# Kernel optimization log

Measured on AMD Instinct MI355X. Metric: run time of the kernel, lower is better.

The kernel has to match this reference:

```python
import jax, jax.numpy as jnp
import numpy as np

EPS = 1e-6        # vn_layers EPS
BN_EPS = 1e-5     # torch BatchNorm eps
NEG = 0.2         # leaky relu negative_slope


def _bcast(v, nd):
    return v.reshape((1, -1) + (1,) * (nd - 2))


def vn_linear_leaky(x, W, D, gamma, beta):
    """VNLinearLeakyReLU: x [B,Cin,3,...], W/D [Cout,Cin] -> [B,Cout,3,...]."""
    p = jnp.einsum('oc,bcv...->bov...', W, x)
    # VNBatchNorm (training-mode batch statistics) on vector norms
    norm = jnp.linalg.norm(p, axis=2) + EPS              # [B,Cout,...]
    axes = (0,) + tuple(range(2, norm.ndim))
    mu = jnp.mean(norm, axis=axes, keepdims=True)
    var = jnp.mean((norm - mu) ** 2, axis=axes, keepdims=True)
    norm_bn = (norm - mu) / jnp.sqrt(var + BN_EPS)
    norm_bn = norm_bn * _bcast(gamma, norm.ndim) + _bcast(beta, norm.ndim)
    p = p / norm[:, :, None] * norm_bn[:, :, None]
    # VN LeakyReLU against learned direction d
    d = jnp.einsum('oc,bcv...->bov...', D, x)
    dot = jnp.sum(p * d, axis=2, keepdims=True)
    mask = (dot >= 0).astype(p.dtype)
    dns = jnp.sum(d * d, axis=2, keepdims=True)
    return NEG * p + (1 - NEG) * (mask * p + (1 - mask) * (p - (dot / (dns + EPS)) * d))


def chnorm(x):
    """channel_equi_vec_normalize: x [B,C,3,...]."""
    n = jnp.linalg.norm(x, axis=2, keepdims=True)        # [B,C,1,...]
    x_dir = x / jnp.maximum(n, 1e-12)
    n_ch = jnp.linalg.norm(n, axis=1, keepdims=True)     # normalize norms over channels
    return x_dir * (n / jnp.maximum(n_ch, 1e-12))


def get_graph_feature(y, k):
    """VN-DGCNN graph feature: y [B,C,3,N] -> [B,2C,3,N,K]."""
    B, C, _, N = y.shape
    yp = jnp.transpose(y, (0, 3, 1, 2))                  # [B,N,C,3]
    flat = yp.reshape(B, N, 3 * C)
    sq = jnp.sum(flat * flat, axis=-1)                   # [B,N]
    inner = jnp.einsum('bnd,bmd->bnm', flat, flat)
    neg_dist = 2 * inner - sq[:, :, None] - sq[:, None, :]
    _, idx = jax.lax.top_k(neg_dist, k)                  # [B,N,K] nearest (incl. self)
    nbr = jax.vmap(lambda pts, ids: pts[ids])(yp, idx)   # [B,N,K,C,3]
    ctr = jnp.broadcast_to(yp[:, :, None], (B, N, k, C, 3))
    feat = jnp.concatenate([nbr - ctr, ctr], axis=3)     # [B,N,K,2C,3]
    return jnp.transpose(feat, (0, 3, 4, 1, 2))


def reference(x, y, Wq, Dq, gq, bq, Wk, Dk, gk, bk, Wv, Dv, gv, bv, k):
    Qx = chnorm(vn_linear_leaky(x, Wq, Dq, gq, bq))      # [B,C,3,N]
    yg = get_graph_feature(y, k)                         # [B,2C,3,N,K]
    Ky = chnorm(vn_linear_leaky(yg, Wk, Dk, gk, bk))     # [B,C,3,N,K]
    Vy = vn_linear_leaky(yg, Wv, Dv, gv, bv)             # [B,C,3,N,K]
    qk = jnp.sum(Ky * Qx[..., None], axis=2)             # [B,C,N,K]
    C = qk.shape[1]
    atten = jax.nn.softmax(qk / jnp.sqrt(jnp.float32(3 * C)), axis=-1)
    return x + jnp.sum(atten[:, :, None] * Vy, axis=-1)  # [B,C,3,N]


def setup_inputs() -> dict:
    key = jax.random.key(0)
    B, C, N, K = 4, 64, 2048, 16
    ks = jax.random.split(key, 8)
    s1 = 1.0 / np.sqrt(C)
    s2 = 1.0 / np.sqrt(2 * C)
    return {
        'x': jax.random.normal(ks[0], (B, C, 3, N), jnp.float32),
        'y': jax.random.normal(ks[1], (B, C, 3, N), jnp.float32),
        'Wq': jax.random.normal(ks[2], (C, C), jnp.float32) * s1,
        'Dq': jax.random.normal(ks[3], (C, C), jnp.float32) * s1,
        'gq': jnp.ones((C,), jnp.float32),
        'bq': jnp.zeros((C,), jnp.float32),
        'Wk': jax.random.normal(ks[4], (C, 2 * C), jnp.float32) * s2,
        'Dk': jax.random.normal(ks[5], (C, 2 * C), jnp.float32) * s2,
        'gk': jnp.ones((C,), jnp.float32),
        'bk': jnp.zeros((C,), jnp.float32),
        'Wv': jax.random.normal(ks[6], (C, 2 * C), jnp.float32) * s2,
        'Dv': jax.random.normal(ks[7], (C, 2 * C), jnp.float32) * s2,
        'gv': jnp.ones((C,), jnp.float32),
        'bv': jnp.zeros((C,), jnp.float32),
        'k': K,
    }
```

## Files before the change

### kernel.cpp

```cpp
#include <hip/hip_runtime.h>
#include <cstdint>
#include <cstddef>

constexpr int B_ = 4, C_ = 64, N_ = 2048, K_ = 16;
constexpr int D3 = 192;
constexpr float EPS_ = 1e-6f, BNE_ = 1e-5f, NEG_ = 0.2f;
constexpr size_t S_ = (size_t)B_ * N_ * D3;

constexpr size_t OFF_PQ  = 0;
constexpr size_t OFF_DQ  = 1*S_;
constexpr size_t OFF_GB  = 2*S_;
constexpr size_t OFF_WK  = 6*S_;
constexpr size_t OFF_WDK = 7*S_;
constexpr size_t OFF_WV  = 8*S_;
constexpr size_t OFF_WDV = 9*S_;
constexpr size_t OFF_SQ  = 10*S_;
constexpr size_t OFF_ST  = OFF_SQ + (size_t)B_*N_;
constexpr size_t OFF_IDX = OFF_ST + 1024;
constexpr size_t OFF_DIST= OFF_IDX + (size_t)B_*N_*K_;

__device__ __forceinline__ float wred_sum(float v) {
  #pragma unroll
  for (int off = 32; off > 0; off >>= 1) v += __shfl_xor(v, off, 64);
  return v;
}

__device__ __forceinline__ void gld_lds16(const float* g, float* l) {
  __builtin_amdgcn_global_load_lds(
      (const __attribute__((address_space(1))) void*)g,
      (__attribute__((address_space(3))) void*)l, 16, 0, 0);
}

__device__ __forceinline__ void vnlk(float& p0, float& p1, float& p2,
                                     float d0, float d1, float d2,
                                     float s, float sh) {
  float n2 = p0*p0 + p1*p1 + p2*p2;
  float norm = __builtin_amdgcn_sqrtf(n2) + EPS_;
  float f = fmaf(norm, s, sh) * __builtin_amdgcn_rcpf(norm);
  p0 *= f; p1 *= f; p2 *= f;
  float dot = p0*d0 + p1*d1 + p2*d2;
  float dns = d0*d0 + d1*d1 + d2*d2;
  float g = (1.f - NEG_) * fminf(dot, 0.f) * __builtin_amdgcn_rcpf(dns + EPS_);
  p0 = fmaf(-g, d0, p0); p1 = fmaf(-g, d1, p1); p2 = fmaf(-g, d2, p2);
}

__device__ __forceinline__ float chnorm_sc(float nc, float nch) {
  return nc * __builtin_amdgcn_rcpf(fmaxf(nc, 1e-12f))
            * __builtin_amdgcn_rcpf(fmaxf(nch, 1e-12f));
}

template<bool PAIR>
__device__ __forceinline__ void do_mm(const float (*ys)[36], const float (*Wl)[129],
                                      float* __restrict__ out0, float* __restrict__ out1,
                                      float* s1s, float* s2s, bool qs,
                                      int og, int ng, int b, int n0, int rs0) {
  float accU[4][2][3] = {};
  float accW[4][2][3] = {};
  #pragma unroll 4
  for (int c = 0; c < 64; ++c) {
    float w1[4], wd[4];
    #pragma unroll
    for (int i = 0; i < 4; ++i) {
      w1[i] = Wl[og*4 + i][c];
      if (PAIR) wd[i] = Wl[og*4 + i][64 + c] - w1[i];
    }
    #pragma unroll
    for (int jj = 0; jj < 2; ++jj)
      #pragma unroll
      for (int v = 0; v < 3; ++v) {
        float yv = ys[c*3 + v][ng*2 + jj];
        #pragma unroll
        for (int i = 0; i < 4; ++i) {
          accU[i][jj][v] = fmaf(w1[i], yv, accU[i][jj][v]);
          if (PAIR) accW[i][jj][v] = fmaf(wd[i], yv, accW[i][jj][v]);
        }
      }
  }
  #pragma unroll
  for (int jj = 0; jj < 2; ++jj) {
    int n = n0 + ng*2 + jj;
    size_t base0 = ((size_t)b*N_ + n)*rs0 + og*12;
    alignas(16) float tmp[12];
    #pragma unroll
    for (int i = 0; i < 4; ++i)
      #pragma unroll
      for (int v = 0; v < 3; ++v) tmp[i*3+v] = accU[i][jj][v];
    float4* dst = (float4*)(out0 + base0);
    dst[0] = ((float4*)tmp)[0]; dst[1] = ((float4*)tmp)[1]; dst[2] = ((float4*)tmp)[2];
    if (PAIR) {
      size_t base1 = ((size_t)b*N_ + n)*D3 + og*12;
      #pragma unroll
      for (int i = 0; i < 4; ++i)
        #pragma unroll
        for (int v = 0; v < 3; ++v) tmp[i*3+v] = accW[i][jj][v];
      float4* dst1 = (float4*)(out1 + base1);
      dst1[0] = ((float4*)tmp)[0]; dst1[1] = ((float4*)tmp)[1]; dst1[2] = ((float4*)tmp)[2];
    }
  }
  if (!PAIR && qs) {
    #pragma unroll
    for (int i = 0; i < 4; ++i) {
      float a = 0.f, b2 = 0.f;
      #pragma unroll
      for (int jj = 0; jj < 2; ++jj) {
        float nn = sqrtf(accU[i][jj][0]*accU[i][jj][0] + accU[i][jj][1]*accU[i][jj][1]
                       + accU[i][jj][2]*accU[i][jj][2]) + EPS_;
        a += nn; b2 += nn*nn;
      }
      atomicAdd(&s1s[og*4 + i], a);
      atomicAdd(&s2s[og*4 + i], b2);
    }
  }
}

__global__ __launch_bounds__(256) void transform_kernel(
    const float* __restrict__ x, const float* __restrict__ y,
    const float* __restrict__ Wq, const float* __restrict__ Dq,
    const float* __restrict__ Wk, const float* __restrict__ Dk,
    const float* __restrict__ Wv, const float* __restrict__ Dv,
    float* __restrict__ ws) {
  __shared__ float ys[D3][36];
  __shared__ float Wl[64][129];
  __shared__ float s1s[64], s2s[64];
  int t = threadIdx.x, n0 = blockIdx.x*32, b = blockIdx.y, z = blockIdx.z;
  const bool isx = (z < 2);
  const float* in = (isx ? x : y) + (size_t)b*D3*N_;
  #pragma unroll
  for (int i = 0; i < 6; ++i) {
    int lin = t + i*256;
    int d = lin >> 3, c4 = (lin & 7)*4;
    *(float4*)&ys[d][c4] = *(const float4*)&in[(size_t)d*N_ + n0 + c4];
  }
  const float* Wg = (z==0)?Wq:(z==1)?Dq:(z==2)?Wk:(z==3)?Dk:(z==4)?Wv:Dv;
  if (isx) { for (int i = t; i < 4096; i += 256) Wl[i>>6][i&63] = Wg[i]; }
  else     { for (int i = t; i < 8192; i += 256) Wl[i>>7][i&127] = Wg[i]; }
  if (z == 0 && t < 64) { s1s[t] = 0.f; s2s[t] = 0.f; }
  __syncthreads();
  if (z == 2 && t < 32) {
    float s = 0.f;
    for (int d = 0; d < D3; ++d) { float v = ys[d][t]; s += v*v; }
    ws[OFF_SQ + (size_t)b*N_ + n0 + t] = s;
  }
  int og = t & 15, ng = t >> 4;
  float* st = ws + OFF_ST;
  if (isx) {
    float* out0 = ws + (z ? OFF_DQ : OFF_PQ);
    do_mm<false>(ys, Wl, out0, nullptr, s1s, s2s, z == 0, og, ng, b, n0, D3);
    if (z == 0) {
      __syncthreads();
      if (t < 64) { atomicAdd(&st[t], s1s[t]); atomicAdd(&st[64 + t], s2s[t]); }
    }
  } else {
    int seg = z - 2;
    float* out0 = ws + OFF_GB + (size_t)seg*192;
    float* out1 = ws + ((z==2)?OFF_WK:(z==3)?OFF_WDK:(z==4)?OFF_WV:OFF_WDV);
    do_mm<true>(ys, Wl, out0, out1, nullptr, nullptr, false, og, ng, b, n0, 768);
  }
}

__global__ __launch_bounds__(256) void dist_kernel(const float* __restrict__ y,
                                                   float* __restrict__ ws,
                                                   int b0, size_t dstride) {
  __shared__ float As[2][2048];
  __shared__ float Bs[2][4096];
  int b = b0 + blockIdx.z;
  const float* yb = y + (size_t)b * D3 * N_;
  const float* sq = ws + OFF_SQ + (size_t)b * N_;
  float* dist = ws + OFF_DIST + dstride * blockIdx.z;
  int t = threadIdx.x;
  int m0 = blockIdx.x * 256, n0 = blockIdx.y * 128;
  int tm = t & 15, tn = t >> 4;

  auto stage = [&](int buf, int dt) {
    #pragma unroll
    for (int j = 0; j < 2; ++j) {
      int idx = j*256 + t;
      gld_lds16(&yb[(size_t)(dt*16 + (idx >> 5))*N_ + n0 + (idx & 31)*4],
                &As[buf][idx*4]);
    }
    #pragma unroll
    for (int j = 0; j < 4; ++j) {
      int idx = j*256 + t;
      gld_lds16(&yb[(size_t)(dt*16 + (idx >> 6))*N_ + m0 + (idx & 63)*4],
                &Bs[buf][idx*4]);
    }
  };

  float acc[8][16] = {};
  stage(0, 0);
  __syncthreads();
  int cur = 0;
  for (int dt = 0; dt < 12; ++dt) {
    if (dt < 11) stage(cur ^ 1, dt + 1);
    const float* Ac = As[cur];
    const float* Bc = Bs[cur];
    #pragma unroll 4
    for (int dd = 0; dd < 16; ++dd) {
      float4 a0 = *(const float4*)&Ac[dd*128 + tn*4];
      float4 a1 = *(const float4*)&Ac[dd*128 + 64 + tn*4];
      float4 b0 = *(const float4*)&Bc[dd*256 + tm*4];
      float4 b1 = *(const float4*)&Bc[dd*256 + 64 + tm*4];
      float4 b2 = *(const float4*)&Bc[dd*256 + 128 + tm*4];
      float4 b3 = *(const float4*)&Bc[dd*256 + 192 + tm*4];
      float an[8] = {a0.x, a0.y, a0.z, a0.w, a1.x, a1.y, a1.z, a1.w};
      float bm[16] = {b0.x, b0.y, b0.z, b0.w, b1.x, b1.y, b1.z, b1.w,
                      b2.x, b2.y, b2.z, b2.w, b3.x, b3.y, b3.z, b3.w};
      #pragma unroll
      for (int j = 0; j < 8; ++j)
        #pragma unroll
        for (int i = 0; i < 16; ++i)
          acc[j][i] = fmaf(an[j], bm[i], acc[j][i]);
    }
    __syncthreads();
    cur ^= 1;
  }
  float smv[16];
  #pragma unroll
  for (int r = 0; r < 4; ++r) {
    float4 s4 = *(const float4*)&sq[m0 + r*64 + tm*4];
    smv[r*4+0] = s4.x; smv[r*4+1] = s4.y; smv[r*4+2] = s4.z; smv[r*4+3] = s4.w;
  }
  #pragma unroll
  for (int j = 0; j < 8; ++j) {
    int n = n0 + ((j < 4) ? (tn*4 + j) : (64 + tn*4 + j - 4));
    float sn = sq[n];
    size_t rowb = (size_t)n*N_ + m0 + tm*4;
    #pragma unroll
    for (int r = 0; r < 4; ++r) {
      float4 rr;
      rr.x = 2.f*acc[j][r*4+0] - sn - smv[r*4+0];
      rr.y = 2.f*acc[j][r*4+1] - sn - smv[r*4+1];
      rr.z = 2.f*acc[j][r*4+2] - sn - smv[r*4+2];
      rr.w = 2.f*acc[j][r*4+3] - sn - smv[r*4+3];
      *(float4*)&dist[rowb + r*64] = rr;
    }
  }
}

__global__ __launch_bounds__(256) void topk_kernel(const float* __restrict__ ws_c,
                                                   int* __restrict__ idxo,
                                                   int b0, size_t dstride) {
  int t = threadIdx.x;
  int w = t >> 6, l = t & 63;
  int n = blockIdx.x*4 + w;
  int b = b0 + blockIdx.y;
  const float* dr = ws_c + OFF_DIST + dstride*blockIdx.y + (size_t)n * N_;
  float v[32];
  #pragma unroll
  for (int j = 0; j < 32; ++j) v[j] = dr[j*64 + l];
  int mine = 0;
  for (int it = 0; it < K_; ++it) {
    float bv = v[0]; int bj = 0;
    #pragma unroll
    for (int j = 1; j < 32; ++j) {
      bool g = v[j] > bv;
      bv = g ? v[j] : bv;
      bj = g ? j : bj;
    }
    int bm = bj*64 + l;
    #pragma unroll
    for (int off = 32; off > 0; off >>= 1) {
      float ov = __shfl_xor(bv, off, 64);
      int   om = __shfl_xor(bm, off, 64);
      if (ov > bv || (ov == bv && om < bm)) { bv = ov; bm = om; }
    }
    if (l == it) mine = bm;
    int wj = bm >> 6, wl = bm & 63;
    #pragma unroll
    for (int j = 0; j < 32; ++j)
      v[j] = (j == wj && l == wl) ? -3.4e38f : v[j];
  }
  if (l < K_) idxo[((size_t)b*N_ + n)*K_ + l] = mine;
}

__global__ __launch_bounds__(256) void kvstats_kernel(float* __restrict__ ws,
                                                      const int* __restrict__ idxp) {
  int t = threadIdx.x, o = t & 63, eg = t >> 6;
  int e0 = blockIdx.x * 128, b = blockIdx.y;
  const float* GB = ws + OFF_GB;
  const float* wK = ws + OFF_WK; const float* wV = ws + OFF_WV;
  int bN = b * N_;
  float k1 = 0.f, k2 = 0.f, v1 = 0.f, v2 = 0.f;
  for (int j = 0; j < 32; ++j) {
    int e = e0 + eg + j*4;
    int n = e >> 4, kk = e & 15;
    int m = idxp[(bN + n)*K_ + kk];
    int rb = (bN + n)*D3 + o*3;
    size_t gb = (size_t)(bN + m)*768 + o*3;
    float p0 = GB[gb] + wK[rb], p1 = GB[gb+1] + wK[rb+1], p2 = GB[gb+2] + wK[rb+2];
    float nk = __builtin_amdgcn_sqrtf(p0*p0 + p1*p1 + p2*p2) + EPS_;
    k1 += nk; k2 += nk*nk;
    float q0 = GB[gb+384] + wV[rb], q1 = GB[gb+385] + wV[rb+1], q2 = GB[gb+386] + wV[rb+2];
    float nv = __builtin_amdgcn_sqrtf(q0*q0 + q1*q1 + q2*q2) + EPS_;
    v1 += nv; v2 += nv*nv;
  }
  __shared__ float red[4][256];
  red[0][t] = k1; red[1][t] = k2; red[2][t] = v1; red[3][t] = v2;
  __syncthreads();
  if (t < 64) {
    float* st = ws + OFF_ST;
    float a = red[0][t] + red[0][t+64] + red[0][t+128] + red[0][t+192];
    atomicAdd(&st[128 + t], a);
    a = red[1][t] + red[1][t+64] + red[1][t+128] + red[1][t+192];
    atomicAdd(&st[192 + t], a);
    a = red[2][t] + red[2][t+64] + red[2][t+128] + red[2][t+192];
    atomicAdd(&st[256 + t], a);
    a = red[3][t] + red[3][t+64] + red[3][t+128] + red[3][t+192];
    atomicAdd(&st[320 + t], a);
  }
}

__global__ __launch_bounds__(256, 2) void final_kernel(const float* __restrict__ x,
                                                       const float* __restrict__ ws_c,
                                                       const int* __restrict__ idxp,
                                                       const float* __restrict__ gq,
                                                       const float* __restrict__ bq,
                                                       const float* __restrict__ gk,
                                                       const float* __restrict__ bk,
                                                       const float* __restrict__ gv,
                                                       const float* __restrict__ bv,
                                                       float* __restrict__ out) {
  const float* pq  = ws_c + OFF_PQ;  const float* dq  = ws_c + OFF_DQ;
  const float* GB  = ws_c + OFF_GB;
  const float* wK  = ws_c + OFF_WK;  const float* wDk = ws_c + OFF_WDK;
  const float* wV  = ws_c + OFF_WV;  const float* wDv = ws_c + OFF_WDV;
  const float* st  = ws_c + OFF_ST;
  int t = threadIdx.x, o = t & 63, w = t >> 6;
  int n0 = blockIdx.x*4, n = n0 + w, b = blockIdx.y;
  int bN = b * N_;
  __shared__ float ob2[192][5];
  float sQ, shQ, sK, shK, sV, shV;
  {
    const float icq = 1.f / (float)(B_ * N_);
    float mu = st[o] * icq;
    float var = fmaxf(st[64+o]*icq - mu*mu, 0.f);
    sQ = gq[o] * rsqrtf(var + BNE_); shQ = bq[o] - mu*sQ;
    const float ick = 1.f / (float)(B_ * N_ * K_);
    mu = st[128+o] * ick;
    var = fmaxf(st[192+o]*ick - mu*mu, 0.f);
    sK = gk[o] * rsqrtf(var + BNE_); shK = bk[o] - mu*sK;
    mu = st[256+o] * ick;
    var = fmaxf(st[320+o]*ick - mu*mu, 0.f);
    sV = gv[o] * rsqrtf(var + BNE_); shV = bv[o] - mu*sV;
  }
  int mi[16];
  {
    const int* ip = idxp + (size_t)(bN + n)*K_;
    int4 a0 = *(const int4*)&ip[0];  mi[0]=a0.x;  mi[1]=a0.y;  mi[2]=a0.z;  mi[3]=a0.w;
    int4 a1 = *(const int4*)&ip[4];  mi[4]=a1.x;  mi[5]=a1.y;  mi[6]=a1.z;  mi[7]=a1.w;
    int4 a2 = *(const int4*)&ip[8];  mi[8]=a2.x;  mi[9]=a2.y;  mi[10]=a2.z; mi[11]=a2.w;
    int4 a3 = *(const int4*)&ip[12]; mi[12]=a3.x; mi[13]=a3.y; mi[14]=a3.z; mi[15]=a3.w;
  }
  int rb = (bN + n)*D3 + o*3;
  float q0 = pq[rb], q1 = pq[rb+1], q2 = pq[rb+2];
  float e0 = dq[rb], e1 = dq[rb+1], e2 = dq[rb+2];
  vnlk(q0, q1, q2, e0, e1, e2, sQ, shQ);
  float qn2 = q0*q0 + q1*q1 + q2*q2;
  float qsc = chnorm_sc(__builtin_amdgcn_sqrtf(qn2),
                        __builtin_amdgcn_sqrtf(wred_sum(qn2)));
  float qx0 = q0*qsc, qx1 = q1*qsc, qx2 = q2*qsc;
  float wk0 = wK[rb],  wk1 = wK[rb+1],  wk2 = wK[rb+2];
  float wdk0= wDk[rb], wdk1= wDk[rb+1], wdk2= wDk[rb+2];
  const float isq = 0.07216878364870323f;
  float qk[16];
  #pragma unroll
  for (int kk = 0; kk < 16; ++kk) {
    size_t gb = (size_t)(bN + mi[kk])*768 + o*3;
    float p0 = GB[gb]     + wk0, p1 = GB[gb+1]   + wk1, p2 = GB[gb+2]   + wk2;
    float f0 = GB[gb+192] + wdk0, f1 = GB[gb+193] + wdk1, f2 = GB[gb+194] + wdk2;
    vnlk(p0, p1, p2, f0, f1, f2, sK, shK);
    float nc2 = p0*p0 + p1*p1 + p2*p2;
    float sc = chnorm_sc(__builtin_amdgcn_sqrtf(nc2),
                         __builtin_amdgcn_sqrtf(wred_sum(nc2)));
    qk[kk] = (p0*qx0 + p1*qx1 + p2*qx2) * (sc * isq);
  }
  float mx = qk[0];
  #pragma unroll
  for (int kk = 1; kk < 16; ++kk) mx = fmaxf(mx, qk[kk]);
  float se = 0.f;
  #pragma unroll
  for (int kk = 0; kk < 16; ++kk) { float e = __expf(qk[kk] - mx); qk[kk] = e; se += e; }
  float inv = __builtin_amdgcn_rcpf(se);
  float wv0 = wV[rb],  wv1 = wV[rb+1],  wv2 = wV[rb+2];
  float wdv0= wDv[rb], wdv1= wDv[rb+1], wdv2= wDv[rb+2];
  float a0 = 0.f, a1 = 0.f, a2 = 0.f;
  #pragma unroll
  for (int kk = 0; kk < 16; ++kk) {
    size_t gb = (size_t)(bN + mi[kk])*768 + o*3;
    float v0 = GB[gb+384] + wv0, v1 = GB[gb+385] + wv1, v2 = GB[gb+386] + wv2;
    float g0 = GB[gb+576] + wdv0, g1 = GB[gb+577] + wdv1, g2 = GB[gb+578] + wdv2;
    vnlk(v0, v1, v2, g0, g1, g2, sV, shV);
    float at = qk[kk] * inv;
    a0 = fmaf(at, v0, a0); a1 = fmaf(at, v1, a1); a2 = fmaf(at, v2, a2);
  }
  ob2[o*3 + 0][w] = a0;
  ob2[o*3 + 1][w] = a1;
  ob2[o*3 + 2][w] = a2;
  __syncthreads();
  if (t < 192) {
    size_t xo = ((size_t)b*D3 + t)*N_ + n0;
    float4 xr = *(const float4*)&x[xo];
    float4 r;
    r.x = xr.x + ob2[t][0]; r.y = xr.y + ob2[t][1];
    r.z = xr.z + ob2[t][2]; r.w = xr.w + ob2[t][3];
    *(float4*)&out[xo] = r;
  }
}

extern "C" void kernel_launch(void* const* d_in, const int* in_sizes, int n_in,
                              void* d_out, int out_size, void* d_ws, size_t ws_size,
                              hipStream_t stream) {
  const float* x  = (const float*)d_in[0];
  const float* y  = (const float*)d_in[1];
  const float* Wq = (const float*)d_in[2];
  const float* Dq = (const float*)d_in[3];
  const float* gq = (const float*)d_in[4];
  const float* bq = (const float*)d_in[5];
  const float* Wk = (const float*)d_in[6];
  const float* Dk = (const float*)d_in[7];
  const float* gk = (const float*)d_in[8];
  const float* bk = (const float*)d_in[9];
  const float* Wv = (const float*)d_in[10];
  const float* Dv = (const float*)d_in[11];
  const float* gv = (const float*)d_in[12];
  const float* bv = (const float*)d_in[13];
  float* ws = (float*)d_ws;
  float* out = (float*)d_out;
  int* idxp = (int*)(ws + OFF_IDX);

  const size_t need = (OFF_DIST + (size_t)B_*N_*N_) * sizeof(float);
  const bool batched = ws_size >= need;

  hipMemsetAsync((void*)(ws + OFF_ST), 0, 1024 * sizeof(float), stream);
  transform_kernel<<<dim3(N_/32, B_, 6), 256, 0, stream>>>(x, y, Wq, Dq, Wk, Dk, Wv, Dv, ws);
  if (batched) {
    dist_kernel<<<dim3(N_/256, N_/128, B_), 256, 0, stream>>>(y, ws, 0, (size_t)N_*N_);
    topk_kernel<<<dim3(N_/4, B_), 256, 0, stream>>>(ws, idxp, 0, (size_t)N_*N_);
  } else {
    for (int b = 0; b < B_; ++b) {
      dist_kernel<<<dim3(N_/256, N_/128, 1), 256, 0, stream>>>(y, ws, b, 0);
      topk_kernel<<<dim3(N_/4, 1), 256, 0, stream>>>(ws, idxp, b, 0);
    }
  }
  kvstats_kernel<<<dim3(N_*K_/128, B_), 256, 0, stream>>>(ws, idxp);
  final_kernel<<<dim3(N_/4, B_), 256, 0, stream>>>(x, ws, idxp, gq, bq, gk, bk, gv, bv, out);
}
```

Baseline: 341.5 us.

## Store gathered neighbor projections as padded bf16 to cut gather bandwidth

Measured after the change: 356.0 us. 1.04x slower.

```diff
diff --git a/kernel.cpp b/kernel.cpp
--- a/kernel.cpp
+++ b/kernel.cpp
@@ -31,6 +31,18 @@
       (__attribute__((address_space(3))) void*)l, 16, 0, 0);
 }
 
+__device__ __forceinline__ unsigned short f2bf(float f) {
+  unsigned int u = __float_as_uint(f);
+  u = u + 0x7FFFu + ((u >> 16) & 1u);
+  return (unsigned short)(u >> 16);
+}
+__device__ __forceinline__ float bfbits(unsigned int hi16) {
+  return __uint_as_float(hi16 << 16);
+}
+__device__ __forceinline__ unsigned int pk2(float a, float b) {
+  return (unsigned int)f2bf(a) | ((unsigned int)f2bf(b) << 16);
+}
+
 __device__ __forceinline__ void vnlk(float& p0, float& p1, float& p2,
                                      float d0, float d1, float d2,
                                      float s, float sh) {
@@ -51,9 +63,11 @@
 
 template<bool PAIR>
 __device__ __forceinline__ void do_mm(const float (*ys)[36], const float (*Wl)[129],
-                                      float* __restrict__ out0, float* __restrict__ out1,
+                                      float* __restrict__ out0,
+                                      unsigned short* __restrict__ outH, int seg,
+                                      float* __restrict__ out1,
                                       float* s1s, float* s2s, bool qs,
-                                      int og, int ng, int b, int n0, int rs0) {
+                                      int og, int ng, int b, int n0) {
   float accU[4][2][3] = {};
   float accW[4][2][3] = {};
   #pragma unroll 4
@@ -79,16 +93,26 @@
   #pragma unroll
   for (int jj = 0; jj < 2; ++jj) {
     int n = n0 + ng*2 + jj;
-    size_t base0 = ((size_t)b*N_ + n)*rs0 + og*12;
-    alignas(16) float tmp[12];
-    #pragma unroll
-    for (int i = 0; i < 4; ++i)
-      #pragma unroll
-      for (int v = 0; v < 3; ++v) tmp[i*3+v] = accU[i][jj][v];
-    float4* dst = (float4*)(out0 + base0);
-    dst[0] = ((float4*)tmp)[0]; dst[1] = ((float4*)tmp)[1]; dst[2] = ((float4*)tmp)[2];
-    if (PAIR) {
+    if (!PAIR) {
+      size_t base0 = ((size_t)b*N_ + n)*D3 + og*12;
+      alignas(16) float tmp[12];
+      #pragma unroll
+      for (int i = 0; i < 4; ++i)
+        #pragma unroll
+        for (int v = 0; v < 3; ++v) tmp[i*3+v] = accU[i][jj][v];
+      float4* dst = (float4*)(out0 + base0);
+      dst[0] = ((float4*)tmp)[0]; dst[1] = ((float4*)tmp)[1]; dst[2] = ((float4*)tmp)[2];
+    } else {
+      size_t hb = ((size_t)b*N_ + n)*1024 + (size_t)seg*256 + og*16;
+      #pragma unroll
+      for (int i = 0; i < 4; ++i) {
+        uint2 pk;
+        pk.x = pk2(accU[i][jj][0], accU[i][jj][1]);
+        pk.y = pk2(accU[i][jj][2], 0.f);
+        *(uint2*)&outH[hb + i*4] = pk;
+      }
       size_t base1 = ((size_t)b*N_ + n)*D3 + og*12;
+      alignas(16) float tmp[12];
       #pragma unroll
       for (int i = 0; i < 4; ++i)
         #pragma unroll
@@ -145,22 +169,22 @@
   float* st = ws + OFF_ST;
   if (isx) {
     float* out0 = ws + (z ? OFF_DQ : OFF_PQ);
-    do_mm<false>(ys, Wl, out0, nullptr, s1s, s2s, z == 0, og, ng, b, n0, D3);
+    do_mm<false>(ys, Wl, out0, nullptr, 0, nullptr, s1s, s2s, z == 0, og, ng, b, n0);
     if (z == 0) {
       __syncthreads();
       if (t < 64) { atomicAdd(&st[t], s1s[t]); atomicAdd(&st[64 + t], s2s[t]); }
     }
   } else {
     int seg = z - 2;
-    float* out0 = ws + OFF_GB + (size_t)seg*192;
+    unsigned short* outH = (unsigned short*)(ws + OFF_GB);
     float* out1 = ws + ((z==2)?OFF_WK:(z==3)?OFF_WDK:(z==4)?OFF_WV:OFF_WDV);
-    do_mm<true>(ys, Wl, out0, out1, nullptr, nullptr, false, og, ng, b, n0, 768);
-  }
-}
-
-__global__ __launch_bounds__(256) void dist_kernel(const float* __restrict__ y,
-                                                   float* __restrict__ ws,
-                                                   int b0, size_t dstride) {
+    do_mm<true>(ys, Wl, nullptr, outH, seg, out1, nullptr, nullptr, false, og, ng, b, n0);
+  }
+}
+
+__global__ __launch_bounds__(256, 1) void dist_kernel(const float* __restrict__ y,
+                                                      float* __restrict__ ws,
+                                                      int b0, size_t dstride) {
   __shared__ float As[2][2048];
   __shared__ float Bs[2][4096];
   int b = b0 + blockIdx.z;
@@ -277,7 +301,7 @@
                                                       const int* __restrict__ idxp) {
   int t = threadIdx.x, o = t & 63, eg = t >> 6;
   int e0 = blockIdx.x * 128, b = blockIdx.y;
-  const float* GB = ws + OFF_GB;
+  const unsigned short* GBH = (const unsigned short*)(ws + OFF_GB);
   const float* wK = ws + OFF_WK; const float* wV = ws + OFF_WV;
   int bN = b * N_;
   float k1 = 0.f, k2 = 0.f, v1 = 0.f, v2 = 0.f;
@@ -286,11 +310,17 @@
     int n = e >> 4, kk = e & 15;
     int m = idxp[(bN + n)*K_ + kk];
     int rb = (bN + n)*D3 + o*3;
-    size_t gb = (size_t)(bN + m)*768 + o*3;
-    float p0 = GB[gb] + wK[rb], p1 = GB[gb+1] + wK[rb+1], p2 = GB[gb+2] + wK[rb+2];
+    size_t hb = (size_t)(bN + m)*1024 + o*4;
+    uint2 hk = *(const uint2*)&GBH[hb];
+    uint2 hv = *(const uint2*)&GBH[hb + 512];
+    float p0 = bfbits(hk.x & 0xFFFF) + wK[rb];
+    float p1 = bfbits(hk.x >> 16)    + wK[rb+1];
+    float p2 = bfbits(hk.y & 0xFFFF) + wK[rb+2];
     float nk = __builtin_amdgcn_sqrtf(p0*p0 + p1*p1 + p2*p2) + EPS_;
     k1 += nk; k2 += nk*nk;
-    float q0 = GB[gb+384] + wV[rb], q1 = GB[gb+385] + wV[rb+1], q2 = GB[gb+386] + wV[rb+2];
+    float q0 = bfbits(hv.x & 0xFFFF) + wV[rb];
+    float q1 = bfbits(hv.x >> 16)    + wV[rb+1];
+    float q2 = bfbits(hv.y & 0xFFFF) + wV[rb+2];
     float nv = __builtin_amdgcn_sqrtf(q0*q0 + q1*q1 + q2*q2) + EPS_;
     v1 += nv; v2 += nv*nv;
   }
@@ -321,7 +351,7 @@
                                                        const float* __restrict__ bv,
                                                        float* __restrict__ out) {
   const float* pq  = ws_c + OFF_PQ;  const float* dq  = ws_c + OFF_DQ;
-  const float* GB  = ws_c + OFF_GB;
+  const unsigned short* GBH = (const unsigned short*)(ws_c + OFF_GB);
   const float* wK  = ws_c + OFF_WK;  const float* wDk = ws_c + OFF_WDK;
   const float* wV  = ws_c + OFF_WV;  const float* wDv = ws_c + OFF_WDV;
   const float* st  = ws_c + OFF_ST;
@@ -365,9 +395,15 @@
   float qk[16];
   #pragma unroll
   for (int kk = 0; kk < 16; ++kk) {
-    size_t gb = (size_t)(bN + mi[kk])*768 + o*3;
-    float p0 = GB[gb]     + wk0, p1 = GB[gb+1]   + wk1, p2 = GB[gb+2]   + wk2;
-    float f0 = GB[gb+192] + wdk0, f1 = GB[gb+193] + wdk1, f2 = GB[gb+194] + wdk2;
+    size_t hb = (size_t)(bN + mi[kk])*1024 + o*4;
+    uint2 h0 = *(const uint2*)&GBH[hb];
+    uint2 h1 = *(const uint2*)&GBH[hb + 256];
+    float p0 = bfbits(h0.x & 0xFFFF) + wk0;
+    float p1 = bfbits(h0.x >> 16)    + wk1;
+    float p2 = bfbits(h0.y & 0xFFFF) + wk2;
+    float f0 = bfbits(h1.x & 0xFFFF) + wdk0;
+    float f1 = bfbits(h1.x >> 16)    + wdk1;
+    float f2 = bfbits(h1.y & 0xFFFF) + wdk2;
     vnlk(p0, p1, p2, f0, f1, f2, sK, shK);
     float nc2 = p0*p0 + p1*p1 + p2*p2;
     float sc = chnorm_sc(__builtin_amdgcn_sqrtf(nc2),
@@ -386,9 +422,15 @@
   float a0 = 0.f, a1 = 0.f, a2 = 0.f;
   #pragma unroll
   for (int kk = 0; kk < 16; ++kk) {
-    size_t gb = (size_t)(bN + mi[kk])*768 + o*3;
-    float v0 = GB[gb+384] + wv0, v1 = GB[gb+385] + wv1, v2 = GB[gb+386] + wv2;
-    float g0 = GB[gb+576] + wdv0, g1 = GB[gb+577] + wdv1, g2 = GB[gb+578] + wdv2;
+    size_t hb = (size_t)(bN + mi[kk])*1024 + o*4;
+    uint2 h2 = *(const uint2*)&GBH[hb + 512];
+    uint2 h3 = *(const uint2*)&GBH[hb + 768];
+    float v0 = bfbits(h2.x & 0xFFFF) + wv0;
+    float v1 = bfbits(h2.x >> 16)    + wv1;
+    float v2 = bfbits(h2.y & 0xFFFF) + wv2;
+    float g0 = bfbits(h3.x & 0xFFFF) + wdv0;
+    float g1 = bfbits(h3.x >> 16)    + wdv1;
+    float g2 = bfbits(h3.y & 0xFFFF) + wdv2;
     vnlk(v0, v1, v2, g0, g1, g2, sV, shV);
     float at = qk[kk] * inv;
     a0 = fmaf(at, v0, a0); a1 = fmaf(at, v1, a1); a2 = fmaf(at, v2, a2);
```
